# Performance work log

Hardware: AMD Instinct MI355X
Metric: run time of the kernel (lower is better)

The kernel has to match this reference:

```python
import jax, jax.numpy as jnp
import numpy as np
from jax import lax

N, L = 4000, 128          # total sentences, sentence length
VOCAB = 50002             # 50000 words + unk + blk
VEC_DIM, POS_DIM = 50, 5
EMB = VEC_DIM + 2 * POS_DIM   # 60
HID = 230
NPOS = 201                # 2*max_pos_length+1
NBAG, BAGSZ = 500, 8
NREL = 25


def setup_inputs() -> dict:
    key = jax.random.key(0)
    ks = jax.random.split(key, 10)
    X = jax.random.randint(ks[0], (N, L), 0, 50000)
    pos1 = jax.random.randint(ks[1], (N, L), 0, NPOS)
    pos2 = jax.random.randint(ks[2], (N, L), 0, NPOS)
    mask = jnp.zeros((N, L), dtype=jnp.int64)       # unused by CNN encoder
    length = jnp.full((N,), L, dtype=jnp.int64)     # unused by CNN encoder
    starts = jnp.arange(NBAG) * BAGSZ
    scope = jnp.stack([starts, starts + BAGSZ], axis=1)  # [NBAG, 2] contiguous bags
    relation = jax.random.randint(ks[3], (NBAG,), 0, NREL)
    word_emb = jax.random.normal(ks[4], (VOCAB, VEC_DIM), jnp.float32) * 0.1
    pos1_emb = jax.random.normal(ks[5], (NPOS, POS_DIM), jnp.float32) * 0.1
    pos2_emb = jax.random.normal(ks[6], (NPOS, POS_DIM), jnp.float32) * 0.1
    conv_w = jax.random.normal(ks[7], (HID, EMB, 3), jnp.float32) * (1.0 / np.sqrt(EMB * 3))
    conv_b = jnp.zeros((HID,), jnp.float32)
    rel_w = jax.random.normal(ks[8], (NREL, HID), jnp.float32) * (1.0 / np.sqrt(HID))
    rel_b = jnp.zeros((NREL,), jnp.float32)
    return {"X": X, "pos1": pos1, "pos2": pos2, "mask": mask, "length": length,
            "scope": scope, "relation": relation, "word_emb": word_emb,
            "pos1_emb": pos1_emb, "pos2_emb": pos2_emb, "conv_w": conv_w,
            "conv_b": conv_b, "rel_w": rel_w, "rel_b": rel_b}


def reference(X, pos1, pos2, mask, length, scope, relation,
              word_emb, pos1_emb, pos2_emb, conv_w, conv_b, rel_w, rel_b):
    # --- word_pos_embedding: gather + concat -> [N, L, EMB]
    emb = jnp.concatenate([word_emb[X], pos1_emb[pos1], pos2_emb[pos2]], axis=-1)
    # --- CNN encoder: conv1d(k=3, same pad) -> max-pool over seq -> relu
    h = lax.conv_general_dilated(
        emb.transpose(0, 2, 1), conv_w, window_strides=(1,), padding='SAME',
        dimension_numbers=('NCH', 'OIH', 'NCH'))  # [N, HID, L]
    h = jax.nn.relu(jnp.max(h + conv_b[None, :, None], axis=2))  # [N, HID]
    # (dropout p=0.0 -> identity)
    # --- ragged per-bag softmax attention pooling (training path, relation given)
    sizes = scope[:, 1] - scope[:, 0]
    bag_ids = jnp.repeat(jnp.arange(NBAG), sizes, total_repeat_length=N)  # [N]
    rel_q = rel_w[relation]                       # [NBAG, HID] attention queries
    logits = jnp.sum(h * rel_q[bag_ids], axis=-1)  # [N]
    m = jax.ops.segment_max(logits, bag_ids, num_segments=NBAG)
    e = jnp.exp(logits - m[bag_ids])
    denom = jax.ops.segment_sum(e, bag_ids, num_segments=NBAG)
    alpha = e / denom[bag_ids]                     # per-bag softmax weights
    bag_rep = jax.ops.segment_sum(alpha[:, None] * h, bag_ids, num_segments=NBAG)  # [NBAG, HID]
    # --- relation classifier
    return bag_rep @ rel_w.T + rel_b               # [NBAG, NREL]
```

## Files before the change

### kernel.cpp

```cpp
#include <hip/hip_runtime.h>
#include <hip/hip_bf16.h>

#define NSENT 4000
#define LSEQ  128
#define VEC   50
#define WSTR  52
#define NVOCAB 50002
#define POS   5
#define EMBD  60
#define HIDD  230
#define HSTR  232
#define NBAG  500
#define NREL  25
#define NTILEP 16
#define KSTEPS 6
#define ESTR  72
#define SLOTS 130
#define SSTR  (SLOTS * ESTR)
#define WBLOCKS 2540

typedef __attribute__((ext_vector_type(8))) short short8;
typedef __attribute__((ext_vector_type(4))) float f32x4;

__device__ __forceinline__ unsigned short f2bf(float f) {
    union { float f; unsigned u; } v; v.f = f;
    unsigned u = v.u + 0x7FFF + ((v.u >> 16) & 1);
    return (unsigned short)(u >> 16);
}

__device__ __forceinline__ unsigned pk(float a, float b) {
    __hip_bfloat162 h = __float22bfloat162_rn(float2{a, b});
    union { __hip_bfloat162 h; unsigned u; } c; c.h = h;
    return c.u;
}

__global__ __launch_bounds__(256) void prep(const float* __restrict__ conv_w,
                                            const float* __restrict__ wemb,
                                            unsigned short* __restrict__ Bfrag,
                                            unsigned short* __restrict__ wbf) {
    int bid = blockIdx.x;
    if (bid < WBLOCKS) {
        int idx = bid * 256 + threadIdx.x;
        if (idx < NVOCAB * 13) {
            int r = idx / 13, cj = (idx % 13) * 4;
            const float* src = wemb + (size_t)r * VEC + cj;
            float2 a = *(const float2*)src;
            float2 b = (cj < 48) ? *(const float2*)(src + 2) : float2{0.f, 0.f};
            uint2 v; v.x = pk(a.x, a.y); v.y = pk(b.x, b.y);
            *(uint2*)(wbf + (size_t)r * WSTR + cj) = v;
        }
    } else {
        int idx = (bid - WBLOCKS) * 256 + threadIdx.x;
        if (idx >= NTILEP * KSTEPS * 64 * 8) return;
        int j    = idx & 7;
        int lane = (idx >> 3) & 63;
        int t    = idx >> 9;
        int ks   = t % KSTEPS;
        int nt   = t / KSTEPS;
        int c    = nt * 16 + (lane & 15);
        int klin = ks * 32 + (lane >> 4) * 8 + j;
        int tap  = klin >> 6;
        int e    = klin & 63;
        float v  = 0.f;
        if (c < HIDD) {
            int eidx = -1;
            if (e < 50)                 eidx = e;
            else if (e >= 52 && e < 56) eidx = 50 + (e - 52);
            else if (e >= 56 && e < 60) eidx = 55 + (e - 56);
            else if (e == 60)           eidx = 54;
            else if (e == 62)           eidx = 59;
            if (eidx >= 0) v = conv_w[(c * EMBD + eidx) * 3 + tap];
        }
        Bfrag[idx] = f2bf(v);
    }
}

__global__ __launch_bounds__(256) void prep_b(const float* __restrict__ conv_w,
                                              unsigned short* __restrict__ Bfrag) {
    int idx = blockIdx.x * 256 + threadIdx.x;
    if (idx >= NTILEP * KSTEPS * 64 * 8) return;
    int j    = idx & 7;
    int lane = (idx >> 3) & 63;
    int t    = idx >> 9;
    int ks   = t % KSTEPS;
    int nt   = t / KSTEPS;
    int c    = nt * 16 + (lane & 15);
    int klin = ks * 32 + (lane >> 4) * 8 + j;
    int tap  = klin >> 6;
    int e    = klin & 63;
    float v  = 0.f;
    if (c < HIDD) {
        int eidx = -1;
        if (e < 50)                 eidx = e;
        else if (e >= 52 && e < 56) eidx = 50 + (e - 52);
        else if (e >= 56 && e < 60) eidx = 55 + (e - 56);
        else if (e == 60)           eidx = 54;
        else if (e == 62)           eidx = 59;
        if (eidx >= 0) v = conv_w[(c * EMBD + eidx) * 3 + tap];
    }
    Bfrag[idx] = f2bf(v);
}

__device__ __forceinline__ void gather_one(
    int s, int tid,
    const int* __restrict__ xS, const int* __restrict__ p1S, const int* __restrict__ p2S,
    const unsigned short* __restrict__ wbf,
    const float* __restrict__ p1emb, const float* __restrict__ p2emb,
    unsigned short* __restrict__ embS)
{
    #pragma unroll
    for (int it = 0; it < (LSEQ * 16) / 512; ++it) {
        int i = tid + it * 512;
        int l = i >> 4, j = i & 15;
        int li = s * LSEQ + l;
        unsigned short* dst = embS + s * SSTR + (l + 1) * ESTR;
        uint2 v;
        if (j < 13) {
            v = *(const uint2*)(wbf + (size_t)xS[li] * WSTR + j * 4);
        } else if (j == 13) {
            const float* p = p1emb + p1S[li] * POS;
            v.x = pk(p[0], p[1]); v.y = pk(p[2], p[3]);
        } else if (j == 14) {
            const float* p = p2emb + p2S[li] * POS;
            v.x = pk(p[0], p[1]); v.y = pk(p[2], p[3]);
        } else {
            float a = p1emb[p1S[li] * POS + 4];
            float b = p2emb[p2S[li] * POS + 4];
            v.x = pk(a, 0.f); v.y = pk(b, 0.f);
        }
        *(uint2*)(dst + (j < 13 ? j * 4 : 52 + (j - 13) * 4)) = v;
    }
}

__device__ __forceinline__ void compute_one(
    const unsigned short* __restrict__ eb, const short8 Bw[2][KSTEPS],
    int m, int quad, int nt0, int lane, int sent_row,
    const float* __restrict__ conv_b, float* __restrict__ H)
{
    float maxv[2][4];
    #pragma unroll
    for (int t = 0; t < 2; ++t)
        #pragma unroll
        for (int r = 0; r < 4; ++r) maxv[t][r] = -1e30f;

    #pragma unroll
    for (int mt = 0; mt < 8; ++mt) {
        short8 A[KSTEPS];
        #pragma unroll
        for (int ks = 0; ks < KSTEPS; ++ks) {
            int tap = ks >> 1;
            int col = (ks & 1) * 32 + quad * 8;
            int row = mt * 16 + m + tap;
            A[ks] = *(const short8*)(eb + row * ESTR + col);
        }
        f32x4 acc[2];
        #pragma unroll
        for (int t = 0; t < 2; ++t) acc[t] = (f32x4){0.f, 0.f, 0.f, 0.f};
        #pragma unroll
        for (int ks = 0; ks < KSTEPS; ++ks)
            #pragma unroll
            for (int t = 0; t < 2; ++t)
                acc[t] = __builtin_amdgcn_mfma_f32_16x16x32_bf16(A[ks], Bw[t][ks], acc[t], 0, 0, 0);
        #pragma unroll
        for (int t = 0; t < 2; ++t)
            #pragma unroll
            for (int r = 0; r < 4; ++r)
                maxv[t][r] = fmaxf(maxv[t][r], acc[t][r]);
    }

    #pragma unroll
    for (int t = 0; t < 2; ++t) {
        float v = fmaxf(fmaxf(maxv[t][0], maxv[t][1]),
                        fmaxf(maxv[t][2], maxv[t][3]));
        v = fmaxf(v, __shfl_xor(v, 16));
        v = fmaxf(v, __shfl_xor(v, 32));
        int c = (nt0 + t) * 16 + lane;
        if (lane < 16 && c < HIDD)
            H[(size_t)sent_row * HSTR + c] = fmaxf(v + conv_b[c], 0.f);
    }
}

__global__ __launch_bounds__(512, 4) void encoder(
    const int*   __restrict__ X,  const int* __restrict__ P1, const int* __restrict__ P2,
    const unsigned short* __restrict__ wbf,
    const float* __restrict__ p1emb, const float* __restrict__ p2emb,
    const unsigned short* __restrict__ Bfrag, const float* __restrict__ conv_b,
    float* __restrict__ H)
{
    __shared__ unsigned short embS[2 * SSTR];
    __shared__ int xS[2 * LSEQ], p1S[2 * LSEQ], p2S[2 * LSEQ];
    const int b2 = blockIdx.x * 2, tid = threadIdx.x;
    const int lane = tid & 63;
    const int wave = __builtin_amdgcn_readfirstlane(tid >> 6);
    const int nt0  = wave * 2;
    const int m    = lane & 15;
    const int quad = lane >> 4;

    short8 Bw[2][KSTEPS];
    #pragma unroll
    for (int t = 0; t < 2; ++t)
        #pragma unroll
        for (int ks = 0; ks < KSTEPS; ++ks)
            Bw[t][ks] = *(const short8*)(Bfrag + ((size_t)((nt0 + t) * KSTEPS + ks) * 64 + lane) * 8);

    #pragma unroll
    for (int it = 0; it < 2; ++it) {
        int i = tid + it * 512;
        if (i < 768) {
            int which = i >> 8, l2 = i & 255;
            const int* src = (which == 0) ? X : (which == 1) ? P1 : P2;
            int v = src[(size_t)b2 * LSEQ + l2];
            int* dst = (which == 0) ? xS : (which == 1) ? p1S : p2S;
            dst[l2] = v;
        } else {
            int t = i - 768;
            if (t < 128) {
                int sent = t >> 6;
                int r = (t & 32) ? (SLOTS - 1) : 0;
                *(unsigned*)(embS + sent * SSTR + r * ESTR + (t & 31) * 2) = 0u;
            }
        }
    }
    __syncthreads();

    gather_one(0, tid, xS, p1S, p2S, wbf, p1emb, p2emb, embS);
    __syncthreads();

    gather_one(1, tid, xS, p1S, p2S, wbf, p1emb, p2emb, embS);
    compute_one(embS, Bw, m, quad, nt0, lane, b2 + 0, conv_b, H);
    __syncthreads();

    compute_one(embS + SSTR, Bw, m, quad, nt0, lane, b2 + 1, conv_b, H);
}

__global__ __launch_bounds__(512, 4) void encoder_f32(
    const int*   __restrict__ X,  const int* __restrict__ P1, const int* __restrict__ P2,
    const float* __restrict__ wemb, const float* __restrict__ p1emb, const float* __restrict__ p2emb,
    const unsigned short* __restrict__ Bfrag, const float* __restrict__ conv_b,
    float* __restrict__ H)
{
    __shared__ unsigned short embS[2 * SSTR];
    __shared__ int xS[2 * LSEQ], p1S[2 * LSEQ], p2S[2 * LSEQ];
    const int b2 = blockIdx.x * 2, tid = threadIdx.x;
    const int lane = tid & 63;
    const int wave = __builtin_amdgcn_readfirstlane(tid >> 6);
    const int nt0  = wave * 2;
    const int m    = lane & 15;
    const int quad = lane >> 4;

    short8 Bw[2][KSTEPS];
    #pragma unroll
    for (int t = 0; t < 2; ++t)
        #pragma unroll
        for (int ks = 0; ks < KSTEPS; ++ks)
            Bw[t][ks] = *(const short8*)(Bfrag + ((size_t)((nt0 + t) * KSTEPS + ks) * 64 + lane) * 8);

    #pragma unroll
    for (int it = 0; it < 2; ++it) {
        int i = tid + it * 512;
        if (i < 768) {
            int which = i >> 8, l2 = i & 255;
            const int* src = (which == 0) ? X : (which == 1) ? P1 : P2;
            int v = src[(size_t)b2 * LSEQ + l2];
            int* dst = (which == 0) ? xS : (which == 1) ? p1S : p2S;
            dst[l2] = v;
        } else {
            int t = i - 768;
            if (t < 128) {
                int sent = t >> 6;
                int r = (t & 32) ? (SLOTS - 1) : 0;
                *(unsigned*)(embS + sent * SSTR + r * ESTR + (t & 31) * 2) = 0u;
            }
        }
    }
    __syncthreads();

    #pragma unroll
    for (int it = 0; it < (2 * LSEQ * 16) / 512; ++it) {
        int i = tid + it * 512;
        int sent = i >> 11, rem = i & 2047;
        int l = rem >> 4, j = rem & 15;
        int li = sent * LSEQ + l;
        unsigned short* dst = embS + sent * SSTR + (l + 1) * ESTR;
        uint2 v;
        if (j < 13) {
            const float* src = wemb + (size_t)xS[li] * VEC + j * 4;
            float2 fa = *(const float2*)(src);
            float a2 = 0.f, a3 = 0.f;
            if (j < 12) { float2 fb = *(const float2*)(src + 2); a2 = fb.x; a3 = fb.y; }
            v.x = pk(fa.x, fa.y); v.y = pk(a2, a3);
        } else if (j == 13) {
            const float* p = p1emb + p1S[li] * POS;
            v.x = pk(p[0], p[1]); v.y = pk(p[2], p[3]);
        } else if (j == 14) {
            const float* p = p2emb + p2S[li] * POS;
            v.x = pk(p[0], p[1]); v.y = pk(p[2], p[3]);
        } else {
            float a = p1emb[p1S[li] * POS + 4];
            float b = p2emb[p2S[li] * POS + 4];
            v.x = pk(a, 0.f); v.y = pk(b, 0.f);
        }
        *(uint2*)(dst + (j < 13 ? j * 4 : 52 + (j - 13) * 4)) = v;
    }
    __syncthreads();

    #pragma unroll 1
    for (int s = 0; s < 2; ++s) {
        const unsigned short* eb = embS + s * SSTR;
        float maxv[2][4];
        #pragma unroll
        for (int t = 0; t < 2; ++t)
            #pragma unroll
            for (int r = 0; r < 4; ++r) maxv[t][r] = -1e30f;

        #pragma unroll
        for (int mt = 0; mt < 8; ++mt) {
            short8 A[KSTEPS];
            #pragma unroll
            for (int ks = 0; ks < KSTEPS; ++ks) {
                int tap = ks >> 1;
                int col = (ks & 1) * 32 + quad * 8;
                int row = mt * 16 + m + tap;
                A[ks] = *(const short8*)(eb + row * ESTR + col);
            }
            f32x4 acc[2];
            #pragma unroll
            for (int t = 0; t < 2; ++t) acc[t] = (f32x4){0.f, 0.f, 0.f, 0.f};
            #pragma unroll
            for (int ks = 0; ks < KSTEPS; ++ks)
                #pragma unroll
                for (int t = 0; t < 2; ++t)
                    acc[t] = __builtin_amdgcn_mfma_f32_16x16x32_bf16(A[ks], Bw[t][ks], acc[t], 0, 0, 0);
            #pragma unroll
            for (int t = 0; t < 2; ++t)
                #pragma unroll
                for (int r = 0; r < 4; ++r)
                    maxv[t][r] = fmaxf(maxv[t][r], acc[t][r]);
        }

        #pragma unroll
        for (int t = 0; t < 2; ++t) {
            float v = fmaxf(fmaxf(maxv[t][0], maxv[t][1]),
                            fmaxf(maxv[t][2], maxv[t][3]));
            v = fmaxf(v, __shfl_xor(v, 16));
            v = fmaxf(v, __shfl_xor(v, 32));
            int c = (nt0 + t) * 16 + lane;
            if (lane < 16 && c < HIDD)
                H[(size_t)(b2 + s) * HSTR + c] = fmaxf(v + conv_b[c], 0.f);
        }
    }
}

__global__ __launch_bounds__(64) void attn(
    const float* __restrict__ H, const float* __restrict__ rel_w, const float* __restrict__ rel_b,
    const int* __restrict__ relation, const int* __restrict__ scope,
    float* __restrict__ out)
{
    const int b = blockIdx.x, lane = threadIdx.x;
    const int start = scope[2 * b];
    int ns = scope[2 * b + 1] - start;
    if (ns > 8) ns = 8;
    const int rel = relation[b];

    float q[4], h[8][4];
    #pragma unroll
    for (int k = 0; k < 4; ++k) {
        int c = lane + 64 * k;
        q[k] = (c < HIDD) ? rel_w[rel * HIDD + c] : 0.f;
    }
    #pragma unroll
    for (int s = 0; s < 8; ++s)
        #pragma unroll
        for (int k = 0; k < 4; ++k) {
            int c = lane + 64 * k;
            h[s][k] = (s < ns && c < HIDD) ? H[(size_t)(start + s) * HSTR + c] : 0.f;
        }

    float logit[8];
    #pragma unroll
    for (int s = 0; s < 8; ++s) {
        float t = q[0] * h[s][0] + q[1] * h[s][1] + q[2] * h[s][2] + q[3] * h[s][3];
        #pragma unroll
        for (int off = 32; off > 0; off >>= 1) t += __shfl_xor(t, off);
        logit[s] = t;
    }

    float mx = -1e30f;
    for (int s = 0; s < ns; ++s) mx = fmaxf(mx, logit[s]);
    float a[8], den = 0.f;
    #pragma unroll
    for (int s = 0; s < 8; ++s) { a[s] = (s < ns) ? expf(logit[s] - mx) : 0.f; den += a[s]; }
    float inv = 1.f / den;

    float rep[4];
    #pragma unroll
    for (int k = 0; k < 4; ++k) {
        float r = 0.f;
        #pragma unroll
        for (int s = 0; s < 8; ++s) r += a[s] * h[s][k];
        rep[k] = r * inv;
    }

    #pragma unroll 5
    for (int g = 0; g < NREL; ++g) {
        float t = 0.f;
        #pragma unroll
        for (int k = 0; k < 4; ++k) {
            int c = lane + 64 * k;
            t += (c < HIDD) ? rel_w[g * HIDD + c] * rep[k] : 0.f;
        }
        #pragma unroll
        for (int off = 32; off > 0; off >>= 1) t += __shfl_xor(t, off);
        if (lane == 0) out[b * NREL + g] = t + rel_b[g];
    }
}

extern "C" void kernel_launch(void* const* d_in, const int* in_sizes, int n_in,
                              void* d_out, int out_size, void* d_ws, size_t ws_size,
                              hipStream_t stream) {
    const int*   X        = (const int*)d_in[0];
    const int*   P1       = (const int*)d_in[1];
    const int*   P2       = (const int*)d_in[2];
    const int*   scope    = (const int*)d_in[5];
    const int*   relation = (const int*)d_in[6];
    const float* wemb     = (const float*)d_in[7];
    const float* p1emb    = (const float*)d_in[8];
    const float* p2emb    = (const float*)d_in[9];
    const float* conv_w   = (const float*)d_in[10];
    const float* conv_b   = (const float*)d_in[11];
    const float* rel_w    = (const float*)d_in[12];
    const float* rel_b    = (const float*)d_in[13];

    char* ws = (char*)d_ws;
    float* H = (float*)ws;
    const size_t offB = (size_t)NSENT * HSTR * 4;
    unsigned short* Bfrag = (unsigned short*)(ws + offB);
    const size_t offW = offB + (size_t)NTILEP * KSTEPS * 64 * 8 * 2;
    unsigned short* wbf = (unsigned short*)(ws + offW);
    const size_t need = offW + (size_t)NVOCAB * WSTR * 2;

    if (ws_size >= need) {
        hipLaunchKernelGGL(prep, dim3(WBLOCKS + 192), dim3(256), 0, stream,
                           conv_w, wemb, Bfrag, wbf);
        hipLaunchKernelGGL(encoder, dim3(NSENT / 2), dim3(512), 0, stream,
                           X, P1, P2, wbf, p1emb, p2emb, Bfrag, conv_b, H);
    } else {
        const int btot = NTILEP * KSTEPS * 64 * 8;
        hipLaunchKernelGGL(prep_b, dim3((btot + 255) / 256), dim3(256), 0, stream,
                           conv_w, Bfrag);
        hipLaunchKernelGGL(encoder_f32, dim3(NSENT / 2), dim3(512), 0, stream,
                           X, P1, P2, wemb, p1emb, p2emb, Bfrag, conv_b, H);
    }
    hipLaunchKernelGGL(attn, dim3(NBAG), dim3(64), 0, stream,
                       H, rel_w, rel_b, relation, scope, (float*)d_out);
}
```

Baseline: 180.0 us.

## Fuse per-bag encoder with attention pooling and classifier in one kernel

The encoder now launches one block per bag (8 sentences) instead of one per sentence pair. Each block loops over the sentences with double-buffered gather and MFMA compute, keeps the pooled hidden vectors in shared memory, and then does the softmax attention and relation classifier in place. This removes the H round trip through global memory and the separate attn launch. The cost is fewer blocks (500 instead of 2000), a longer serial chain per block, and more shared memory. It also assumes bags are contiguous, of size 8, and aligned to the block index.

```diff
diff --git a/kernel.cpp b/kernel.cpp
--- a/kernel.cpp
+++ b/kernel.cpp
@@ -12,6 +12,7 @@
 #define HSTR  232
 #define NBAG  500
 #define NREL  25
+#define BAGSZ 8
 #define NTILEP 16
 #define KSTEPS 6
 #define ESTR  72
@@ -102,18 +103,17 @@
 }
 
 __device__ __forceinline__ void gather_one(
-    int s, int tid,
+    unsigned short* __restrict__ slab, int s, int tid,
     const int* __restrict__ xS, const int* __restrict__ p1S, const int* __restrict__ p2S,
     const unsigned short* __restrict__ wbf,
-    const float* __restrict__ p1emb, const float* __restrict__ p2emb,
-    unsigned short* __restrict__ embS)
+    const float* __restrict__ p1emb, const float* __restrict__ p2emb)
 {
     #pragma unroll
     for (int it = 0; it < (LSEQ * 16) / 512; ++it) {
         int i = tid + it * 512;
         int l = i >> 4, j = i & 15;
         int li = s * LSEQ + l;
-        unsigned short* dst = embS + s * SSTR + (l + 1) * ESTR;
+        unsigned short* dst = slab + (l + 1) * ESTR;
         uint2 v;
         if (j < 13) {
             v = *(const uint2*)(wbf + (size_t)xS[li] * WSTR + j * 4);
@@ -132,10 +132,10 @@
     }
 }
 
-__device__ __forceinline__ void compute_one(
+__device__ __forceinline__ void compute_one_lds(
     const unsigned short* __restrict__ eb, const short8 Bw[2][KSTEPS],
-    int m, int quad, int nt0, int lane, int sent_row,
-    const float* __restrict__ conv_b, float* __restrict__ H)
+    int m, int quad, int nt0, int lane,
+    const float* __restrict__ conv_b, float* __restrict__ hrow)
 {
     float maxv[2][4];
     #pragma unroll
@@ -176,20 +176,25 @@
         v = fmaxf(v, __shfl_xor(v, 32));
         int c = (nt0 + t) * 16 + lane;
         if (lane < 16 && c < HIDD)
-            H[(size_t)sent_row * HSTR + c] = fmaxf(v + conv_b[c], 0.f);
-    }
-}
-
-__global__ __launch_bounds__(512, 4) void encoder(
+            hrow[c] = fmaxf(v + conv_b[c], 0.f);
+    }
+}
+
+__global__ __launch_bounds__(512, 4) void encoder_bag(
     const int*   __restrict__ X,  const int* __restrict__ P1, const int* __restrict__ P2,
     const unsigned short* __restrict__ wbf,
     const float* __restrict__ p1emb, const float* __restrict__ p2emb,
     const unsigned short* __restrict__ Bfrag, const float* __restrict__ conv_b,
-    float* __restrict__ H)
+    const int* __restrict__ relation, const int* __restrict__ scope,
+    const float* __restrict__ rel_w, const float* __restrict__ rel_b,
+    float* __restrict__ out)
 {
     __shared__ unsigned short embS[2 * SSTR];
-    __shared__ int xS[2 * LSEQ], p1S[2 * LSEQ], p2S[2 * LSEQ];
-    const int b2 = blockIdx.x * 2, tid = threadIdx.x;
+    __shared__ int xS[BAGSZ * LSEQ], p1S[BAGSZ * LSEQ], p2S[BAGSZ * LSEQ];
+    __shared__ float hS[BAGSZ][HSTR];
+    __shared__ float lgS[BAGSZ];
+    __shared__ float repS[HSTR];
+    const int b = blockIdx.x, tid = threadIdx.x;
     const int lane = tid & 63;
     const int wave = __builtin_amdgcn_readfirstlane(tid >> 6);
     const int nt0  = wave * 2;
@@ -204,33 +209,78 @@
             Bw[t][ks] = *(const short8*)(Bfrag + ((size_t)((nt0 + t) * KSTEPS + ks) * 64 + lane) * 8);
 
     #pragma unroll
-    for (int it = 0; it < 2; ++it) {
+    for (int it = 0; it < 6; ++it) {
         int i = tid + it * 512;
-        if (i < 768) {
-            int which = i >> 8, l2 = i & 255;
-            const int* src = (which == 0) ? X : (which == 1) ? P1 : P2;
-            int v = src[(size_t)b2 * LSEQ + l2];
-            int* dst = (which == 0) ? xS : (which == 1) ? p1S : p2S;
-            dst[l2] = v;
-        } else {
-            int t = i - 768;
-            if (t < 128) {
-                int sent = t >> 6;
-                int r = (t & 32) ? (SLOTS - 1) : 0;
-                *(unsigned*)(embS + sent * SSTR + r * ESTR + (t & 31) * 2) = 0u;
-            }
-        }
+        int arr = i >> 10, off = i & 1023;
+        const int* src = (arr == 0) ? X : (arr == 1) ? P1 : P2;
+        int v = src[(size_t)b * (BAGSZ * LSEQ) + off];
+        int* dst = (arr == 0) ? xS : (arr == 1) ? p1S : p2S;
+        dst[off] = v;
+    }
+    if (tid < 128) {
+        int sb = tid >> 6;
+        int r = (tid & 32) ? (SLOTS - 1) : 0;
+        *(unsigned*)(embS + sb * SSTR + r * ESTR + (tid & 31) * 2) = 0u;
     }
     __syncthreads();
 
-    gather_one(0, tid, xS, p1S, p2S, wbf, p1emb, p2emb, embS);
+    gather_one(embS, 0, tid, xS, p1S, p2S, wbf, p1emb, p2emb);
     __syncthreads();
 
-    gather_one(1, tid, xS, p1S, p2S, wbf, p1emb, p2emb, embS);
-    compute_one(embS, Bw, m, quad, nt0, lane, b2 + 0, conv_b, H);
+    #pragma unroll 1
+    for (int s = 0; s < BAGSZ; ++s) {
+        if (s < BAGSZ - 1)
+            gather_one(embS + ((s + 1) & 1) * SSTR, s + 1, tid, xS, p1S, p2S,
+                       wbf, p1emb, p2emb);
+        compute_one_lds(embS + (s & 1) * SSTR, Bw, m, quad, nt0, lane,
+                        conv_b, &hS[s][0]);
+        __syncthreads();
+    }
+
+    const int start = scope[2 * b];
+    int ns = scope[2 * b + 1] - start;
+    if (ns > BAGSZ) ns = BAGSZ;
+    const int rel = relation[b];
+    {
+        float t = 0.f;
+        #pragma unroll
+        for (int k = 0; k < 4; ++k) {
+            int c = lane + 64 * k;
+            t += (c < HIDD) ? hS[wave][c] * rel_w[rel * HIDD + c] : 0.f;
+        }
+        #pragma unroll
+        for (int off = 32; off > 0; off >>= 1) t += __shfl_xor(t, off);
+        if (lane == 0) lgS[wave] = t;
+    }
     __syncthreads();
 
-    compute_one(embS + SSTR, Bw, m, quad, nt0, lane, b2 + 1, conv_b, H);
+    float mx = -1e30f;
+    #pragma unroll
+    for (int s = 0; s < BAGSZ; ++s) if (s < ns) mx = fmaxf(mx, lgS[s]);
+    float aw[BAGSZ]; float den = 0.f;
+    #pragma unroll
+    for (int s = 0; s < BAGSZ; ++s) { aw[s] = (s < ns) ? expf(lgS[s] - mx) : 0.f; den += aw[s]; }
+    float inv = 1.f / den;
+    if (tid < HIDD) {
+        float r = 0.f;
+        #pragma unroll
+        for (int s = 0; s < BAGSZ; ++s) r += aw[s] * hS[s][tid];
+        repS[tid] = r * inv;
+    }
+    __syncthreads();
+
+    #pragma unroll 1
+    for (int g = wave; g < NREL; g += 8) {
+        float t = 0.f;
+        #pragma unroll
+        for (int k = 0; k < 4; ++k) {
+            int c = lane + 64 * k;
+            t += (c < HIDD) ? repS[c] * rel_w[g * HIDD + c] : 0.f;
+        }
+        #pragma unroll
+        for (int off = 32; off > 0; off >>= 1) t += __shfl_xor(t, off);
+        if (lane == 0) out[b * NREL + g] = t + rel_b[g];
+    }
 }
 
 __global__ __launch_bounds__(512, 4) void encoder_f32(
@@ -442,15 +492,16 @@
     if (ws_size >= need) {
         hipLaunchKernelGGL(prep, dim3(WBLOCKS + 192), dim3(256), 0, stream,
                            conv_w, wemb, Bfrag, wbf);
-        hipLaunchKernelGGL(encoder, dim3(NSENT / 2), dim3(512), 0, stream,
-                           X, P1, P2, wbf, p1emb, p2emb, Bfrag, conv_b, H);
+        hipLaunchKernelGGL(encoder_bag, dim3(NBAG), dim3(512), 0, stream,
+                           X, P1, P2, wbf, p1emb, p2emb, Bfrag, conv_b,
+                           relation, scope, rel_w, rel_b, (float*)d_out);
     } else {
         const int btot = NTILEP * KSTEPS * 64 * 8;
         hipLaunchKernelGGL(prep_b, dim3((btot + 255) / 256), dim3(256), 0, stream,
                            conv_w, Bfrag);
         hipLaunchKernelGGL(encoder_f32, dim3(NSENT / 2), dim3(512), 0, stream,
                            X, P1, P2, wemb, p1emb, p2emb, Bfrag, conv_b, H);
-    }
-    hipLaunchKernelGGL(attn, dim3(NBAG), dim3(64), 0, stream,
-                       H, rel_w, rel_b, relation, scope, (float*)d_out);
-}
+        hipLaunchKernelGGL(attn, dim3(NBAG), dim3(64), 0, stream,
+                           H, rel_w, rel_b, relation, scope, (float*)d_out);
+    }
+}
```

Result: faster. 157.6 us (-12.4%).
